# Performance work log

Hardware: AMD Instinct MI355X
Metric: run time of the kernel (lower is better)

The kernel has to match this reference:

```python
import jax, jax.numpy as jnp
import numpy as np

EPS = 1e-8  # torch F.cosine_similarity default eps

N, M, PLANES = 4096, 4096, 512


def setup_inputs() -> dict:
    key = jax.random.key(0)
    k1, k2, k3, k4 = jax.random.split(key, 4)
    pre = jax.random.normal(k1, (N, PLANES), dtype=jnp.float32)
    cur = jax.random.normal(k2, (M, PLANES), dtype=jnp.float32)
    adj = jax.random.uniform(k3, (N, M), dtype=jnp.float32)
    stdv = 1.0 / np.sqrt(PLANES)
    weight = jax.random.uniform(k4, (PLANES, PLANES), dtype=jnp.float32,
                                minval=-stdv, maxval=stdv)
    return {"pre": pre, "cur": cur, "adj": adj, "weight": weight}


def reference(pre, cur, adj, weight):
    # --- GraphConvolution ---
    pre_w = pre @ weight            # [N, P]
    cur_w = cur @ weight            # [M, P]
    pre_h = adj @ cur_w             # [N, P]  adj_norm @ cur_
    cur_h = adj.T @ pre_w           # [M, P]  adj_t_norm @ pre_

    # --- edge_update: tan(cosine_similarity) for all (i, j) pairs, fused ---
    # cosine_similarity(x, y) = (x . y) / (max(||x||, eps) * max(||y||, eps))
    pre_norm = jnp.maximum(jnp.linalg.norm(pre_h, axis=1, keepdims=True), EPS)
    cur_norm = jnp.maximum(jnp.linalg.norm(cur_h, axis=1, keepdims=True), EPS)
    pre_n = pre_h / pre_norm        # [N, P]
    cur_n = cur_h / cur_norm        # [M, P]
    cos = pre_n @ cur_n.T           # [N, M]
    adj_out = jnp.tan(cos)          # [N, M]
    score = adj_out.reshape(-1)     # [N*M], row-major == i * M + j ordering
    return (score, adj_out)
```

## Files before the change

kernel.cpp:

```cpp
#include <hip/hip_runtime.h>

typedef unsigned short ushort_t;
typedef __attribute__((ext_vector_type(8))) short short8;
typedef __attribute__((ext_vector_type(4))) float f32x4;

__device__ __forceinline__ ushort_t f2bf(float x) {
  union { float f; unsigned u; } v; v.f = x;
  unsigned r = v.u + 0x7fffu + ((v.u >> 16) & 1u);
  return (ushort_t)(r >> 16);
}
__device__ __forceinline__ float bf2f(ushort_t h) {
  union { unsigned u; float f; } v; v.u = ((unsigned)h) << 16;
  return v.f;
}

__device__ __forceinline__ void async_cp16(const ushort_t* g, ushort_t* lds) {
  __builtin_amdgcn_global_load_lds(
      (const __attribute__((address_space(1))) unsigned int*)g,
      (__attribute__((address_space(3))) unsigned int*)lds, 16, 0, 0);
}

template <int MT, int NT, int BKT, int EPI>
__device__ __forceinline__ void gemm_core(
    const ushort_t* __restrict__ A, int lda,
    const ushort_t* __restrict__ B, int ldb,
    int K,
    ushort_t* sA, ushort_t* sB,
    ushort_t* Cb, float* Cf0, float* Cf1, int ldc,
    const float* __restrict__ ip, const float* __restrict__ ic) {
  constexpr int MI = MT / 32, NI = NT / 32, KU = BKT / 32;
  constexpr int LPR = BKT / 8;
  constexpr int RPC = 256 / LPR;
  static_assert(RPC % 8 == 0, "row&7 must be per-lane constant");
  const int t = threadIdx.x;
  const int wave = t >> 6, lane = t & 63;
  const int lm = lane & 15, lq = lane >> 4;
  const int wr = wave >> 1, wc = wave & 1;

  f32x4 acc[MI][NI] = {};

  const int srow = t / LPR;
  const int gseg = (t % LPR) ^ (srow & 7);
  const ushort_t* ga = A + (size_t)srow * lda + gseg * 8;
  const ushort_t* gb = B + (size_t)srow * ldb + gseg * 8;
  ushort_t* sA0 = sA + wave * 512;
  ushort_t* sB0 = sB + wave * 512;

  const int sw = lm & 7;

  for (int k0 = 0; k0 < K; k0 += BKT) {
#pragma unroll
    for (int j = 0; j < MT / RPC; j++)
      async_cp16(ga + k0 + (size_t)j * RPC * lda, sA0 + j * 2048);
#pragma unroll
    for (int j = 0; j < NT / RPC; j++)
      async_cp16(gb + k0 + (size_t)j * RPC * ldb, sB0 + j * 2048);
    __syncthreads();

#pragma unroll
    for (int ku = 0; ku < KU; ku++) {
      short8 af[MI], bf4[NI];
#pragma unroll
      for (int i = 0; i < MI; i++)
        af[i] = *(const short8*)(sA + (wr * (MT / 2) + i * 16 + lm) * BKT +
                                 ((ku * 4 + lq) ^ sw) * 8);
#pragma unroll
      for (int i = 0; i < NI; i++)
        bf4[i] = *(const short8*)(sB + (wc * (NT / 2) + i * 16 + lm) * BKT +
                                  ((ku * 4 + lq) ^ sw) * 8);
#pragma unroll
      for (int mt = 0; mt < MI; mt++)
#pragma unroll
        for (int nt = 0; nt < NI; nt++)
          acc[mt][nt] = __builtin_amdgcn_mfma_f32_16x16x32_bf16(
              af[mt], bf4[nt], acc[mt][nt], 0, 0, 0);
    }
    __syncthreads();
  }

#pragma unroll
  for (int mt = 0; mt < MI; mt++) {
    int rb = wr * (MT / 2) + mt * 16 + lq * 4;
#pragma unroll
    for (int nt = 0; nt < NI; nt++) {
      int c = wc * (NT / 2) + nt * 16 + lm;
#pragma unroll
      for (int r = 0; r < 4; r++) {
        size_t idx = (size_t)(rb + r) * ldc + c;
        if (EPI == 1) {
          Cb[idx] = f2bf(acc[mt][nt][r]);
        } else {
          float v = __tanf(acc[mt][nt][r] * ip[rb + r] * ic[c]);
          Cf0[idx] = v;
          Cf1[idx] = v;
        }
      }
    }
  }
}

__global__ __launch_bounds__(256) void convT(
    const float* __restrict__ in, ushort_t* __restrict__ outn,
    ushort_t* __restrict__ outt, int n) {
  __shared__ float tile[64][65];
  const int t = threadIdx.x;
  const int r0 = blockIdx.y * 64, c0 = blockIdx.x * 64;
  const int cr = t >> 4;
  const int cc = (t & 15) * 4;
#pragma unroll
  for (int p = 0; p < 4; p++) {
    int r = cr + p * 16;
    float4 v = *(const float4*)(in + (size_t)(r0 + r) * n + c0 + cc);
    tile[r][cc + 0] = v.x; tile[r][cc + 1] = v.y;
    tile[r][cc + 2] = v.z; tile[r][cc + 3] = v.w;
    ushort4 o;
    o.x = f2bf(v.x); o.y = f2bf(v.y); o.z = f2bf(v.z); o.w = f2bf(v.w);
    *(ushort4*)(outn + (size_t)(r0 + r) * n + c0 + cc) = o;
  }
  __syncthreads();
#pragma unroll
  for (int p = 0; p < 4; p++) {
    int r = cr + p * 16;
    ushort4 o;
    o.x = f2bf(tile[cc + 0][r]); o.y = f2bf(tile[cc + 1][r]);
    o.z = f2bf(tile[cc + 2][r]); o.w = f2bf(tile[cc + 3][r]);
    *(ushort4*)(outt + (size_t)(c0 + r) * n + r0 + cc) = o;
  }
}

__global__ __launch_bounds__(256) void xcvt(
    const float* __restrict__ pre, const float* __restrict__ cur,
    ushort_t* __restrict__ xbf) {
  const size_t i = ((size_t)blockIdx.x * 256 + threadIdx.x) * 8;
  const float* src =
      (i < (size_t)4096 * 512) ? (pre + i) : (cur + (i - (size_t)4096 * 512));
  float4 a = *(const float4*)(src);
  float4 b = *(const float4*)(src + 4);
  short8 o;
  o[0] = (short)f2bf(a.x); o[1] = (short)f2bf(a.y);
  o[2] = (short)f2bf(a.z); o[3] = (short)f2bf(a.w);
  o[4] = (short)f2bf(b.x); o[5] = (short)f2bf(b.y);
  o[6] = (short)f2bf(b.z); o[7] = (short)f2bf(b.w);
  *(short8*)(xbf + i) = o;
}

__global__ __launch_bounds__(256) void k1_gemm(
    const ushort_t* __restrict__ wt_t, const ushort_t* __restrict__ xbf,
    ushort_t* __restrict__ pw_t) {
  __shared__ __align__(16) ushort_t sA[64 * 64];
  __shared__ __align__(16) ushort_t sB[128 * 64];
  const int bm = blockIdx.x & 7, bn = blockIdx.x >> 3;
  const ushort_t* A = wt_t + (size_t)bm * 64 * 512;
  const ushort_t* B = xbf + (size_t)bn * 128 * 512;
  ushort_t* C = pw_t + (size_t)bm * 64 * 8192 + bn * 128;
  gemm_core<64, 128, 64, 1>(A, 512, B, 512, 512, sA, sB, C, nullptr, nullptr,
                            8192, nullptr, nullptr);
}

__global__ __launch_bounds__(256) void k2_gemm(
    const ushort_t* __restrict__ adj, const ushort_t* __restrict__ adj_t,
    const ushort_t* __restrict__ pw_t, ushort_t* __restrict__ pn) {
  __shared__ __align__(16) ushort_t sA[128 * 128];
  __shared__ __align__(16) ushort_t sB[64 * 128];
  const int b = blockIdx.x;
  const int xcd = b & 7, i = b >> 3;
  const int half = xcd & 1;
  const int bm = ((xcd >> 1) << 3) | (i & 7);
  const int bn = i >> 3;
  const ushort_t* A = (half ? adj_t : adj) + (size_t)bm * 128 * 4096;
  const ushort_t* B = pw_t + (size_t)bn * 64 * 8192 + (half ? 0 : 4096);
  ushort_t* C = pn + (half ? (size_t)4096 * 512 : 0) +
                (size_t)bm * 128 * 512 + bn * 64;
  gemm_core<128, 64, 128, 1>(A, 4096, B, 8192, 4096, sA, sB, C, nullptr,
                             nullptr, 512, nullptr, nullptr);
}

__global__ __launch_bounds__(256) void invnorm_kernel(
    const ushort_t* __restrict__ pn, float* __restrict__ invn) {
  const int t = threadIdx.x;
  const int wave = t >> 6, lane = t & 63;
  const size_t row = (size_t)blockIdx.x * 4 + wave;
  const ushort_t* p = pn + row * 512 + lane * 8;
  short8 v = *(const short8*)p;
  float s = 0.f;
#pragma unroll
  for (int i = 0; i < 8; i++) {
    float f = bf2f((ushort_t)v[i]);
    s += f * f;
  }
#pragma unroll
  for (int off = 32; off > 0; off >>= 1) s += __shfl_xor(s, off, 64);
  if (lane == 0) invn[row] = 1.0f / fmaxf(sqrtf(s), 1e-8f);
}

__global__ __launch_bounds__(256) void k3_gemm(
    const ushort_t* __restrict__ pn, const float* __restrict__ invn,
    float* __restrict__ out) {
  __shared__ __align__(16) ushort_t sA[128 * 64];
  __shared__ __align__(16) ushort_t sB[128 * 64];
  const int b = blockIdx.x;
  const int xcd = b & 7, i = b >> 3;
  const int bm = (xcd << 2) | (i & 3);
  const int bn = i >> 2;
  const ushort_t* A = pn + (size_t)bm * 128 * 512;
  const ushort_t* B = pn + (size_t)4096 * 512 + (size_t)bn * 128 * 512;
  float* C0 = out + (size_t)bm * 128 * 4096 + bn * 128;
  gemm_core<128, 128, 64, 2>(A, 512, B, 512, 512, sA, sB, nullptr, C0,
                             C0 + (size_t)4096 * 4096, 4096,
                             invn + bm * 128, invn + 4096 + bn * 128);
}

extern "C" void kernel_launch(void* const* d_in, const int* in_sizes, int n_in,
                              void* d_out, int out_size, void* d_ws,
                              size_t ws_size, hipStream_t stream) {
  const float* pre = (const float*)d_in[0];
  const float* cur = (const float*)d_in[1];
  const float* adj = (const float*)d_in[2];
  const float* wt  = (const float*)d_in[3];
  float* out = (float*)d_out;

  ushort_t* adj_bf = (ushort_t*)d_ws;
  ushort_t* adj_t  = adj_bf + (size_t)4096 * 4096;
  ushort_t* pw_t   = adj_t + (size_t)4096 * 4096;
  ushort_t* pn     = pw_t + (size_t)512 * 8192;
  ushort_t* wt_t   = pn + (size_t)8192 * 512;
  ushort_t* wt_bf  = wt_t + (size_t)512 * 512;
  float*    invn   = (float*)(wt_bf + (size_t)512 * 512);
  ushort_t* xbf    = (ushort_t*)(invn + 8192);

  convT<<<dim3(64, 64), 256, 0, stream>>>(adj, adj_bf, adj_t, 4096);
  convT<<<dim3(8, 8), 256, 0, stream>>>(wt, wt_bf, wt_t, 512);
  xcvt<<<2048, 256, 0, stream>>>(pre, cur, xbf);
  k1_gemm<<<512, 256, 0, stream>>>(wt_t, xbf, pw_t);
  k2_gemm<<<512, 256, 0, stream>>>(adj_bf, adj_t, pw_t, pn);
  invnorm_kernel<<<2048, 256, 0, stream>>>(pn, invn);
  k3_gemm<<<1024, 256, 0, stream>>>(pn, invn, out);
}
```

Before: 304.5 us.

## Double-buffer LDS tiles in GEMM core to overlap async loads with MFMA

Turns the shared GEMM core into a two-stage pipeline. The next K tile is issued into a second LDS buffer right after the barrier while MFMAs consume the current buffer, which removes the trailing barrier and exposes load latency less. k2's K-tile shrinks from 128 to 64 so the doubled buffers fit, and k3's block-to-tile mapping drops the XCD-aware swizzle for a plain row-major order. The cost is twice the LDS per block, which may reduce occupancy, and possibly worse L2 locality in k3.

```diff
diff --git a/kernel.cpp b/kernel.cpp
--- a/kernel.cpp
+++ b/kernel.cpp
@@ -21,7 +21,7 @@
 }
 
 template <int MT, int NT, int BKT, int EPI>
-__device__ __forceinline__ void gemm_core(
+__device__ __forceinline__ void gemm_core2(
     const ushort_t* __restrict__ A, int lda,
     const ushort_t* __restrict__ B, int ldb,
     int K,
@@ -31,6 +31,8 @@
   constexpr int MI = MT / 32, NI = NT / 32, KU = BKT / 32;
   constexpr int LPR = BKT / 8;
   constexpr int RPC = 256 / LPR;
+  constexpr int ASZ = MT * BKT, BSZ = NT * BKT;
+  static_assert(LPR == 8, "swizzle assumes 8 segs per row");
   static_assert(RPC % 8 == 0, "row&7 must be per-lane constant");
   const int t = threadIdx.x;
   const int wave = t >> 6, lane = t & 63;
@@ -43,30 +45,36 @@
   const int gseg = (t % LPR) ^ (srow & 7);
   const ushort_t* ga = A + (size_t)srow * lda + gseg * 8;
   const ushort_t* gb = B + (size_t)srow * ldb + gseg * 8;
-  ushort_t* sA0 = sA + wave * 512;
-  ushort_t* sB0 = sB + wave * 512;
-
   const int sw = lm & 7;
 
+  auto stage = [&](int k0, int buf) {
+    ushort_t* dA = sA + buf * ASZ + wave * 512;
+    ushort_t* dB = sB + buf * BSZ + wave * 512;
+#pragma unroll
+    for (int j = 0; j < MT / RPC; j++)
+      async_cp16(ga + k0 + (size_t)j * RPC * lda, dA + j * 2048);
+#pragma unroll
+    for (int j = 0; j < NT / RPC; j++)
+      async_cp16(gb + k0 + (size_t)j * RPC * ldb, dB + j * 2048);
+  };
+
+  stage(0, 0);
+  int cur = 0;
   for (int k0 = 0; k0 < K; k0 += BKT) {
-#pragma unroll
-    for (int j = 0; j < MT / RPC; j++)
-      async_cp16(ga + k0 + (size_t)j * RPC * lda, sA0 + j * 2048);
-#pragma unroll
-    for (int j = 0; j < NT / RPC; j++)
-      async_cp16(gb + k0 + (size_t)j * RPC * ldb, sB0 + j * 2048);
     __syncthreads();
-
+    if (k0 + BKT < K) stage(k0 + BKT, cur ^ 1);
+    const ushort_t* cA = sA + cur * ASZ;
+    const ushort_t* cB = sB + cur * BSZ;
 #pragma unroll
     for (int ku = 0; ku < KU; ku++) {
       short8 af[MI], bf4[NI];
 #pragma unroll
       for (int i = 0; i < MI; i++)
-        af[i] = *(const short8*)(sA + (wr * (MT / 2) + i * 16 + lm) * BKT +
+        af[i] = *(const short8*)(cA + (wr * (MT / 2) + i * 16 + lm) * BKT +
                                  ((ku * 4 + lq) ^ sw) * 8);
 #pragma unroll
       for (int i = 0; i < NI; i++)
-        bf4[i] = *(const short8*)(sB + (wc * (NT / 2) + i * 16 + lm) * BKT +
+        bf4[i] = *(const short8*)(cB + (wc * (NT / 2) + i * 16 + lm) * BKT +
                                   ((ku * 4 + lq) ^ sw) * 8);
 #pragma unroll
       for (int mt = 0; mt < MI; mt++)
@@ -75,7 +83,7 @@
           acc[mt][nt] = __builtin_amdgcn_mfma_f32_16x16x32_bf16(
               af[mt], bf4[nt], acc[mt][nt], 0, 0, 0);
     }
-    __syncthreads();
+    cur ^= 1;
   }
 
 #pragma unroll
@@ -147,21 +155,21 @@
 __global__ __launch_bounds__(256) void k1_gemm(
     const ushort_t* __restrict__ wt_t, const ushort_t* __restrict__ xbf,
     ushort_t* __restrict__ pw_t) {
-  __shared__ __align__(16) ushort_t sA[64 * 64];
-  __shared__ __align__(16) ushort_t sB[128 * 64];
+  __shared__ __align__(16) ushort_t sA[2 * 64 * 64];
+  __shared__ __align__(16) ushort_t sB[2 * 128 * 64];
   const int bm = blockIdx.x & 7, bn = blockIdx.x >> 3;
   const ushort_t* A = wt_t + (size_t)bm * 64 * 512;
   const ushort_t* B = xbf + (size_t)bn * 128 * 512;
   ushort_t* C = pw_t + (size_t)bm * 64 * 8192 + bn * 128;
-  gemm_core<64, 128, 64, 1>(A, 512, B, 512, 512, sA, sB, C, nullptr, nullptr,
-                            8192, nullptr, nullptr);
+  gemm_core2<64, 128, 64, 1>(A, 512, B, 512, 512, sA, sB, C, nullptr, nullptr,
+                             8192, nullptr, nullptr);
 }
 
 __global__ __launch_bounds__(256) void k2_gemm(
     const ushort_t* __restrict__ adj, const ushort_t* __restrict__ adj_t,
     const ushort_t* __restrict__ pw_t, ushort_t* __restrict__ pn) {
-  __shared__ __align__(16) ushort_t sA[128 * 128];
-  __shared__ __align__(16) ushort_t sB[64 * 128];
+  __shared__ __align__(16) ushort_t sA[2 * 128 * 64];
+  __shared__ __align__(16) ushort_t sB[2 * 64 * 64];
   const int b = blockIdx.x;
   const int xcd = b & 7, i = b >> 3;
   const int half = xcd & 1;
@@ -171,7 +179,7 @@
   const ushort_t* B = pw_t + (size_t)bn * 64 * 8192 + (half ? 0 : 4096);
   ushort_t* C = pn + (half ? (size_t)4096 * 512 : 0) +
                 (size_t)bm * 128 * 512 + bn * 64;
-  gemm_core<128, 64, 128, 1>(A, 4096, B, 8192, 4096, sA, sB, C, nullptr,
+  gemm_core2<128, 64, 64, 1>(A, 4096, B, 8192, 4096, sA, sB, C, nullptr,
                              nullptr, 512, nullptr, nullptr);
 }
 
@@ -196,18 +204,15 @@
 __global__ __launch_bounds__(256) void k3_gemm(
     const ushort_t* __restrict__ pn, const float* __restrict__ invn,
     float* __restrict__ out) {
-  __shared__ __align__(16) ushort_t sA[128 * 64];
-  __shared__ __align__(16) ushort_t sB[128 * 64];
-  const int b = blockIdx.x;
-  const int xcd = b & 7, i = b >> 3;
-  const int bm = (xcd << 2) | (i & 3);
-  const int bn = i >> 2;
+  __shared__ __align__(16) ushort_t sA[2 * 128 * 64];
+  __shared__ __align__(16) ushort_t sB[2 * 128 * 64];
+  const int bm = blockIdx.x & 31, bn = blockIdx.x >> 5;
   const ushort_t* A = pn + (size_t)bm * 128 * 512;
   const ushort_t* B = pn + (size_t)4096 * 512 + (size_t)bn * 128 * 512;
   float* C0 = out + (size_t)bm * 128 * 4096 + bn * 128;
-  gemm_core<128, 128, 64, 2>(A, 512, B, 512, 512, sA, sB, nullptr, C0,
-                             C0 + (size_t)4096 * 4096, 4096,
-                             invn + bm * 128, invn + 4096 + bn * 128);
+  gemm_core2<128, 128, 64, 2>(A, 512, B, 512, 512, sA, sB, nullptr, C0,
+                              C0 + (size_t)4096 * 4096, 4096,
+                              invn + bm * 128, invn + 4096 + bn * 128);
 }
 
 extern "C" void kernel_launch(void* const* d_in, const int* in_sizes, int n_in,
```

After: 311.5 us. 2.3% more time.
